# Kernel optimization log

Measured on AMD Instinct MI355X. Metric: run time of the kernel, lower is better.

The kernel has to match this reference:

```python
import jax, jax.numpy as jnp
import numpy as np

N, D, V = 2048, 128, 131072
B, T = 8, 256
U_DECAY, X_DECAY, THR = 0.97, 0.97, 0.02


def _ln(z, eps=1e-6):
    # row-wise layernorm matching torch: std with ddof=1 (unbiased)
    m = z.mean(-1, keepdims=True)
    s = jnp.sqrt(((z - m) ** 2).sum(-1, keepdims=True) / (z.shape[-1] - 1))
    return (z - m) / (s + eps)


def setup_inputs() -> dict:
    key = jax.random.key(0)
    k = jax.random.split(key, 5)
    E = jax.random.normal(k[0], (D, N), dtype=jnp.float32) / N ** 0.5
    Dx = jax.random.normal(k[1], (N, D), dtype=jnp.float32) / D ** 0.5
    Dy = jax.random.normal(k[2], (N, D), dtype=jnp.float32) / D ** 0.5
    token_emb = jax.random.normal(k[3], (V, D), dtype=jnp.float32) / D ** 0.5
    tokens = jax.random.randint(k[4], (B, T), 0, V)
    return {"E": E, "Dx": Dx, "Dy": Dy, "token_emb": token_emb, "tokens": tokens}


def reference(E, Dx, Dy, token_emb, tokens):
    Bc, Tc = tokens.shape
    n, d = Dx.shape[0], Dx.shape[1]
    x0 = jnp.zeros((Bc, n), dtype=E.dtype)
    rho0 = jnp.zeros((Bc, d, n), dtype=E.dtype)

    def cell(carry, tok):
        x, rho = carry
        v_prev = token_emb[tok]                             # [B,d]
        xt = X_DECAY * x + v_prev @ Dx.T                    # [B,n]
        xt = xt / (jnp.abs(xt).sum(-1, keepdims=True) + 1e-6)
        thr = THR * xt.max(-1, keepdims=True)
        xt = jnp.where(xt > thr, xt, 0.0)                   # sparsifying threshold
        a_star = jnp.einsum('bdn,bn->bd', rho, xt)          # fast-weight read
        y_core = _ln(a_star) @ Dy.T                         # ln_before_Dy=True -> [B,n]
        yt = jnp.maximum(y_core, 0.0) * jnp.maximum(xt, 0.0)
        v_star = _ln(yt @ E.T)                              # [B,d]
        rho = U_DECAY * (rho + v_prev[:, :, None] * xt[:, None, :])  # rank-1 update + decay
        return (xt, rho), v_star

    (_, _), v_seq = jax.lax.scan(cell, (x0, rho0), tokens.T)  # v_seq: [T,B,d]
    return jnp.transpose(v_seq, (1, 0, 2))                    # [B,T,d]
```

## Files before the change

### kernel.cpp

```cpp
#include <hip/hip_runtime.h>

#define T_SEQ 256
#define N_DIM 2048
#define D_DIM 128
#define B_BATCH 8

__global__ __launch_bounds__(128) void k_gather(const float* __restrict__ emb,
                                                const int* __restrict__ toks,
                                                float* __restrict__ Vp) {
  int r = blockIdx.x;
  int d = threadIdx.x;
  int tok = toks[r];
  Vp[(long)r * D_DIM + d] = emb[(long)tok * D_DIM + d];
}

__global__ __launch_bounds__(256) void k_zero(float* __restrict__ p, long n4) {
  long i = (long)blockIdx.x * blockDim.x + threadIdx.x;
  if (i < n4) ((float4*)p)[i] = make_float4(0.f, 0.f, 0.f, 0.f);
}

template <int FUSE>
__global__ __launch_bounds__(256) void k_gemm_abT(
    const float* __restrict__ A, const float* __restrict__ Bm, float* __restrict__ C,
    int M, int N, int K, long sA, long sB, long sC, const float* __restrict__ Xr) {
  constexpr int BM = 64, BN = 64, BK = 16;
  A += (long)blockIdx.z * sA;
  Bm += (long)blockIdx.z * sB;
  C += (long)blockIdx.z * sC;
  const float* Xp = Xr ? Xr + (long)blockIdx.z * sC : nullptr;

  __shared__ float As[BK][BM + 4];
  __shared__ float Bs[BK][BN + 4];
  int tid = threadIdx.x;
  int tx = tid & 15, ty = tid >> 4;
  int row0 = blockIdx.y * BM, col0 = blockIdx.x * BN;
  float acc[4][4] = {};

  for (int k0 = 0; k0 < K; k0 += BK) {
#pragma unroll
    for (int i = 0; i < 4; i++) {
      int idx = tid + i * 256;
      int m = idx >> 4;
      int k = idx & 15;
      As[k][m] = A[(long)(row0 + m) * K + k0 + k];
      Bs[k][m] = Bm[(long)(col0 + m) * K + k0 + k];
    }
    __syncthreads();
#pragma unroll
    for (int k = 0; k < BK; k++) {
      float a[4], b[4];
#pragma unroll
      for (int i = 0; i < 4; i++) a[i] = As[k][ty * 4 + i];
#pragma unroll
      for (int j = 0; j < 4; j++) b[j] = Bs[k][tx * 4 + j];
#pragma unroll
      for (int i = 0; i < 4; i++)
#pragma unroll
        for (int j = 0; j < 4; j++) acc[i][j] += a[i] * b[j];
    }
    __syncthreads();
  }
#pragma unroll
  for (int i = 0; i < 4; i++) {
    long r = row0 + ty * 4 + i;
    long c = col0 + tx * 4;
    long off = r * (long)N + c;
    float4 v = make_float4(acc[i][0], acc[i][1], acc[i][2], acc[i][3]);
    if (FUSE) {
      float4 xv = *(const float4*)(Xp + off);
      v.x = fmaxf(v.x, 0.f) * fmaxf(xv.x, 0.f);
      v.y = fmaxf(v.y, 0.f) * fmaxf(xv.y, 0.f);
      v.z = fmaxf(v.z, 0.f) * fmaxf(xv.z, 0.f);
      v.w = fmaxf(v.w, 0.f) * fmaxf(xv.w, 0.f);
    }
    *(float4*)(C + off) = v;
  }
}

template <int TRI>
__global__ __launch_bounds__(256) void k_gemm_abT_splitk(
    const float* __restrict__ A, const float* __restrict__ Bm, float* __restrict__ C,
    int M, int N, int K, int KS, long sA, long sB, long sC) {
  constexpr int BM = 64, BN = 64, BK = 16;
  int bz = blockIdx.z;
  int batch = bz / KS, ks = bz - batch * KS;
  A += (long)batch * sA;
  Bm += (long)batch * sB;
  C += (long)batch * sC;
  int row0 = blockIdx.y * BM, col0 = blockIdx.x * BN;
  if (TRI && col0 > row0) return;
  int kLen = K / KS, k0beg = ks * kLen;

  __shared__ float As[BK][BM + 4];
  __shared__ float Bs[BK][BN + 4];
  int tid = threadIdx.x;
  int tx = tid & 15, ty = tid >> 4;
  float acc[4][4] = {};

  for (int k0 = k0beg; k0 < k0beg + kLen; k0 += BK) {
#pragma unroll
    for (int i = 0; i < 4; i++) {
      int idx = tid + i * 256;
      int m = idx >> 4;
      int k = idx & 15;
      As[k][m] = A[(long)(row0 + m) * K + k0 + k];
      Bs[k][m] = Bm[(long)(col0 + m) * K + k0 + k];
    }
    __syncthreads();
#pragma unroll
    for (int k = 0; k < BK; k++) {
      float a[4], b[4];
#pragma unroll
      for (int i = 0; i < 4; i++) a[i] = As[k][ty * 4 + i];
#pragma unroll
      for (int j = 0; j < 4; j++) b[j] = Bs[k][tx * 4 + j];
#pragma unroll
      for (int i = 0; i < 4; i++)
#pragma unroll
        for (int j = 0; j < 4; j++) acc[i][j] += a[i] * b[j];
    }
    __syncthreads();
  }
#pragma unroll
  for (int i = 0; i < 4; i++) {
    long r = row0 + ty * 4 + i;
    long c = col0 + tx * 4;
    float* cp = C + r * (long)N + c;
#pragma unroll
    for (int j = 0; j < 4; j++) unsafeAtomicAdd(cp + j, acc[i][j]);
  }
}

template <int CTRL>
__device__ __forceinline__ float dpp_mov(float v) {
  return __int_as_float(
      __builtin_amdgcn_update_dpp(0, __float_as_int(v), CTRL, 0xF, 0xF, true));
}

__device__ __forceinline__ void wave_reduce_sum_max63(float& s, float& m) {
  s += dpp_mov<0x111>(s);  m = fmaxf(m, dpp_mov<0x111>(m));
  s += dpp_mov<0x112>(s);  m = fmaxf(m, dpp_mov<0x112>(m));
  s += dpp_mov<0x114>(s);  m = fmaxf(m, dpp_mov<0x114>(m));
  s += dpp_mov<0x118>(s);  m = fmaxf(m, dpp_mov<0x118>(m));
  s += dpp_mov<0x142>(s);  m = fmaxf(m, dpp_mov<0x142>(m));
  s += dpp_mov<0x143>(s);  m = fmaxf(m, dpp_mov<0x143>(m));
}

__global__ __launch_bounds__(256) void k_scan(const float* __restrict__ P,
                                              float* __restrict__ X) {
  int b = blockIdx.x;
  int tid = threadIdx.x;
  int wave = tid >> 6;
  int lane = tid & 63;
  __shared__ float red[2][4][2];

  const float4* Pv = (const float4*)(P + (long)b * T_SEQ * N_DIM);
  float4* Xv = (float4*)(X + (long)b * T_SEQ * N_DIM);
  const int ROWQ = N_DIM / 4;
  const long o0 = (long)tid * 2, o1 = o0 + 1;

  float x[8];
#pragma unroll
  for (int j = 0; j < 8; j++) x[j] = 0.f;

  auto rowOff = [&](int t) { return (long)(t < T_SEQ ? t : T_SEQ - 1) * ROWQ; };

  auto step = [&](const float4& v0, const float4& v1, int t) {
    float z[8];
    z[0] = 0.97f * x[0] + v0.x;
    z[1] = 0.97f * x[1] + v0.y;
    z[2] = 0.97f * x[2] + v0.z;
    z[3] = 0.97f * x[3] + v0.w;
    z[4] = 0.97f * x[4] + v1.x;
    z[5] = 0.97f * x[5] + v1.y;
    z[6] = 0.97f * x[6] + v1.z;
    z[7] = 0.97f * x[7] + v1.w;
    float s0 = fabsf(z[0]) + fabsf(z[4]);
    float s1 = fabsf(z[1]) + fabsf(z[5]);
    float s2 = fabsf(z[2]) + fabsf(z[6]);
    float s3 = fabsf(z[3]) + fabsf(z[7]);
    float m0 = fmaxf(z[0], z[4]);
    float m1 = fmaxf(z[1], z[5]);
    float m2 = fmaxf(z[2], z[6]);
    float m3 = fmaxf(z[3], z[7]);
    float s = (s0 + s1) + (s2 + s3);
    float m = fmaxf(fmaxf(m0, m1), fmaxf(m2, m3));
    wave_reduce_sum_max63(s, m);
    int par = t & 1;
    if (lane == 63) {
      red[par][wave][0] = s;
      red[par][wave][1] = m;
    }
    __syncthreads();
    float S = (red[par][0][0] + red[par][1][0]) + (red[par][2][0] + red[par][3][0]);
    float M = fmaxf(fmaxf(red[par][0][1], red[par][1][1]),
                    fmaxf(red[par][2][1], red[par][3][1]));
    float inv = 1.f / (S + 1e-6f);
    float thr = 0.02f * M;
#pragma unroll
    for (int j = 0; j < 8; j++) x[j] = (z[j] > thr) ? z[j] * inv : 0.f;
    long rb = (long)t * ROWQ;
    Xv[rb + o0] = make_float4(x[0], x[1], x[2], x[3]);
    Xv[rb + o1] = make_float4(x[4], x[5], x[6], x[7]);
  };

  float4 A0 = Pv[rowOff(0) + o0], A1 = Pv[rowOff(0) + o1];
  float4 B0 = Pv[rowOff(1) + o0], B1 = Pv[rowOff(1) + o1];
  float4 C0 = Pv[rowOff(2) + o0], C1 = Pv[rowOff(2) + o1];
  float4 D0, D1;

  for (int t = 0; t < T_SEQ; t += 4) {
    D0 = Pv[rowOff(t + 3) + o0];
    D1 = Pv[rowOff(t + 3) + o1];
    step(A0, A1, t);
    A0 = Pv[rowOff(t + 4) + o0];
    A1 = Pv[rowOff(t + 4) + o1];
    step(B0, B1, t + 1);
    B0 = Pv[rowOff(t + 5) + o0];
    B1 = Pv[rowOff(t + 5) + o1];
    step(C0, C1, t + 2);
    C0 = Pv[rowOff(t + 6) + o0];
    C1 = Pv[rowOff(t + 6) + o1];
    step(D0, D1, t + 3);
  }
}

__global__ __launch_bounds__(128) void k_astar(const float* __restrict__ S,
                                               const float* __restrict__ Vp,
                                               float* __restrict__ A) {
  int bx = blockIdx.x;
  int b = bx >> 8, t = bx & 255;
  int d = threadIdx.x;
  const float* Sb = S + ((long)b * T_SEQ + t) * T_SEQ;
  const float* Vb = Vp + (long)b * T_SEQ * D_DIM;
  float acc = 0.f;
  float w = 1.f;
  for (int s = t - 1; s >= 0; s--) {
    w *= 0.97f;
    acc += w * Sb[s] * Vb[(long)s * D_DIM + d];
  }
  A[((long)b * T_SEQ + t) * D_DIM + d] = acc;
}

__global__ __launch_bounds__(64) void k_ln(const float* __restrict__ In,
                                           float* __restrict__ Out) {
  long base = (long)blockIdx.x * D_DIM;
  int lane = threadIdx.x;
  float a = In[base + lane];
  float b = In[base + lane + 64];
  float s = a + b;
#pragma unroll
  for (int off = 32; off >= 1; off >>= 1) s += __shfl_xor(s, off);
  float m = s * (1.f / 128.f);
  float da = a - m, db = b - m;
  float v = da * da + db * db;
#pragma unroll
  for (int off = 32; off >= 1; off >>= 1) v += __shfl_xor(v, off);
  float sd = sqrtf(v * (1.f / 127.f));
  float invs = 1.f / (sd + 1e-6f);
  Out[base + lane] = da * invs;
  Out[base + lane + 64] = db * invs;
}

extern "C" void kernel_launch(void* const* d_in, const int* in_sizes, int n_in,
                              void* d_out, int out_size, void* d_ws, size_t ws_size,
                              hipStream_t stream) {
  const float* E = (const float*)d_in[0];
  const float* Dx = (const float*)d_in[1];
  const float* Dy = (const float*)d_in[2];
  const float* emb = (const float*)d_in[3];
  const int* toks = (const int*)d_in[4];
  float* out = (float*)d_out;

  char* ws = (char*)d_ws;
  const size_t MB = 1u << 20;
  float* Vp = (float*)(ws + 0 * MB);
  float* P = (float*)(ws + 1 * MB);
  float* X = (float*)(ws + 17 * MB);
  float* S = (float*)(ws + 33 * MB);
  float* A = (float*)(ws + 35 * MB);
  float* LnA = (float*)(ws + 36 * MB);
  float* U = (float*)(ws + 37 * MB);
  float* Yt = P;

  const int R = B_BATCH * T_SEQ;

  k_gather<<<R, D_DIM, 0, stream>>>(emb, toks, Vp);
  k_gemm_abT<0><<<dim3(N_DIM / 64, R / 64, 1), 256, 0, stream>>>(
      Vp, Dx, P, R, N_DIM, D_DIM, 0, 0, 0, nullptr);
  k_scan<<<B_BATCH, 256, 0, stream>>>(P, X);
  k_zero<<<(B_BATCH * T_SEQ * T_SEQ / 4 + 255) / 256, 256, 0, stream>>>(
      S, B_BATCH * T_SEQ * T_SEQ / 4);
  k_zero<<<(R * D_DIM / 4 + 255) / 256, 256, 0, stream>>>(U, R * D_DIM / 4);
  k_gemm_abT_splitk<1><<<dim3(T_SEQ / 64, T_SEQ / 64, B_BATCH * 4), 256, 0, stream>>>(
      X, X, S, T_SEQ, T_SEQ, N_DIM, 4,
      (long)T_SEQ * N_DIM, (long)T_SEQ * N_DIM, (long)T_SEQ * T_SEQ);
  k_astar<<<R, D_DIM, 0, stream>>>(S, Vp, A);
  k_ln<<<R, 64, 0, stream>>>(A, LnA);
  k_gemm_abT<1><<<dim3(N_DIM / 64, R / 64, 1), 256, 0, stream>>>(
      LnA, Dy, Yt, R, N_DIM, D_DIM, 0, 0, 0, X);
  k_gemm_abT_splitk<0><<<dim3(D_DIM / 64, R / 64, 8), 256, 0, stream>>>(
      Yt, E, U, R, D_DIM, N_DIM, 8, 0, 0, 0);
  k_ln<<<R, 64, 0, stream>>>(U, out);
}
```

Before: 362.2 us.

## Fuse a_star with layernorm, merge zero kernels, raise S split-K to 8

Merges the a_star accumulation and its row layernorm into one kernel using DPP wave reductions, which drops the intermediate A buffer write and read plus one launch. U is moved next to S so a single zero kernel clears both buffers. The split-K factor for the X·Xᵀ gemm doubles to 8 for more parallelism, at the cost of more atomic adds. Compiler memory barriers are added in the scan loop to keep prefetch loads ahead of each step.

Result: no change. 361.7 us (-0.1%).

```diff
diff --git a/kernel.cpp b/kernel.cpp
--- a/kernel.cpp
+++ b/kernel.cpp
@@ -144,6 +144,16 @@
   s += dpp_mov<0x118>(s);  m = fmaxf(m, dpp_mov<0x118>(m));
   s += dpp_mov<0x142>(s);  m = fmaxf(m, dpp_mov<0x142>(m));
   s += dpp_mov<0x143>(s);  m = fmaxf(m, dpp_mov<0x143>(m));
+}
+
+__device__ __forceinline__ float wave_sum63(float s) {
+  s += dpp_mov<0x111>(s);
+  s += dpp_mov<0x112>(s);
+  s += dpp_mov<0x114>(s);
+  s += dpp_mov<0x118>(s);
+  s += dpp_mov<0x142>(s);
+  s += dpp_mov<0x143>(s);
+  return s;
 }
 
 __global__ __launch_bounds__(256) void k_scan(const float* __restrict__ P,
@@ -207,30 +217,37 @@
   float4 A0 = Pv[rowOff(0) + o0], A1 = Pv[rowOff(0) + o1];
   float4 B0 = Pv[rowOff(1) + o0], B1 = Pv[rowOff(1) + o1];
   float4 C0 = Pv[rowOff(2) + o0], C1 = Pv[rowOff(2) + o1];
+  asm volatile("" ::: "memory");
   float4 D0, D1;
 
   for (int t = 0; t < T_SEQ; t += 4) {
     D0 = Pv[rowOff(t + 3) + o0];
     D1 = Pv[rowOff(t + 3) + o1];
+    asm volatile("" ::: "memory");
     step(A0, A1, t);
     A0 = Pv[rowOff(t + 4) + o0];
     A1 = Pv[rowOff(t + 4) + o1];
+    asm volatile("" ::: "memory");
     step(B0, B1, t + 1);
     B0 = Pv[rowOff(t + 5) + o0];
     B1 = Pv[rowOff(t + 5) + o1];
+    asm volatile("" ::: "memory");
     step(C0, C1, t + 2);
     C0 = Pv[rowOff(t + 6) + o0];
     C1 = Pv[rowOff(t + 6) + o1];
+    asm volatile("" ::: "memory");
     step(D0, D1, t + 3);
   }
 }
 
-__global__ __launch_bounds__(128) void k_astar(const float* __restrict__ S,
-                                               const float* __restrict__ Vp,
-                                               float* __restrict__ A) {
+__global__ __launch_bounds__(128) void k_astar_ln(const float* __restrict__ S,
+                                                  const float* __restrict__ Vp,
+                                                  float* __restrict__ LnA) {
   int bx = blockIdx.x;
   int b = bx >> 8, t = bx & 255;
   int d = threadIdx.x;
+  int wave = d >> 6, lane = d & 63;
+  __shared__ float redS[2], redV[2];
   const float* Sb = S + ((long)b * T_SEQ + t) * T_SEQ;
   const float* Vb = Vp + (long)b * T_SEQ * D_DIM;
   float acc = 0.f;
@@ -239,7 +256,16 @@
     w *= 0.97f;
     acc += w * Sb[s] * Vb[(long)s * D_DIM + d];
   }
-  A[((long)b * T_SEQ + t) * D_DIM + d] = acc;
+  float s1 = wave_sum63(acc);
+  if (lane == 63) redS[wave] = s1;
+  __syncthreads();
+  float mean = (redS[0] + redS[1]) * (1.f / 128.f);
+  float dv = acc - mean;
+  float v = wave_sum63(dv * dv);
+  if (lane == 63) redV[wave] = v;
+  __syncthreads();
+  float sd = sqrtf((redV[0] + redV[1]) * (1.f / 127.f));
+  LnA[((long)b * T_SEQ + t) * D_DIM + d] = dv / (sd + 1e-6f);
 }
 
 __global__ __launch_bounds__(64) void k_ln(const float* __restrict__ In,
@@ -278,9 +304,8 @@
   float* P = (float*)(ws + 1 * MB);
   float* X = (float*)(ws + 17 * MB);
   float* S = (float*)(ws + 33 * MB);
-  float* A = (float*)(ws + 35 * MB);
+  float* U = (float*)(ws + 35 * MB);
   float* LnA = (float*)(ws + 36 * MB);
-  float* U = (float*)(ws + 37 * MB);
   float* Yt = P;
 
   const int R = B_BATCH * T_SEQ;
@@ -289,14 +314,11 @@
   k_gemm_abT<0><<<dim3(N_DIM / 64, R / 64, 1), 256, 0, stream>>>(
       Vp, Dx, P, R, N_DIM, D_DIM, 0, 0, 0, nullptr);
   k_scan<<<B_BATCH, 256, 0, stream>>>(P, X);
-  k_zero<<<(B_BATCH * T_SEQ * T_SEQ / 4 + 255) / 256, 256, 0, stream>>>(
-      S, B_BATCH * T_SEQ * T_SEQ / 4);
-  k_zero<<<(R * D_DIM / 4 + 255) / 256, 256, 0, stream>>>(U, R * D_DIM / 4);
-  k_gemm_abT_splitk<1><<<dim3(T_SEQ / 64, T_SEQ / 64, B_BATCH * 4), 256, 0, stream>>>(
-      X, X, S, T_SEQ, T_SEQ, N_DIM, 4,
+  k_zero<<<768, 256, 0, stream>>>(S, 3L * MB / 16);
+  k_gemm_abT_splitk<1><<<dim3(T_SEQ / 64, T_SEQ / 64, B_BATCH * 8), 256, 0, stream>>>(
+      X, X, S, T_SEQ, T_SEQ, N_DIM, 8,
       (long)T_SEQ * N_DIM, (long)T_SEQ * N_DIM, (long)T_SEQ * T_SEQ);
-  k_astar<<<R, D_DIM, 0, stream>>>(S, Vp, A);
-  k_ln<<<R, 64, 0, stream>>>(A, LnA);
+  k_astar_ln<<<R, D_DIM, 0, stream>>>(S, Vp, LnA);
   k_gemm_abT<1><<<dim3(N_DIM / 64, R / 64, 1), 256, 0, stream>>>(
       LnA, Dy, Yt, R, N_DIM, D_DIM, 0, 0, 0, X);
   k_gemm_abT_splitk<0><<<dim3(D_DIM / 64, R / 64, 8), 256, 0, stream>>>(
```
